# Optimization experiments

Measured on AMD Instinct MI355X. Metric: run time of the kernel, lower is better.

## Reference

```python
import jax, jax.numpy as jnp
import numpy as np

N_COARSE = 64  # n_coarse samples per ray
EPS = 1e-8
DELTA_INF = 1e10


def setup_inputs() -> dict:
    key = jax.random.key(0)
    ks = jax.random.split(key, 8)
    B, H = 16384, 256
    near = 2.0 + jax.random.uniform(ks[0], (B, 1), dtype=jnp.float32)
    far = 6.0 + jax.random.uniform(ks[1], (B, 1), dtype=jnp.float32)
    center = jax.random.normal(ks[2], (B, 3), dtype=jnp.float32)
    direction = jax.random.normal(ks[3], (B, 3), dtype=jnp.float32)
    direction = direction / jnp.linalg.norm(direction, axis=-1, keepdims=True)
    # stand-in NeRF field: 3 -> 256 -> 256 -> 4 MLP (rgb + sigma)
    W1 = jax.random.normal(ks[4], (3, H), dtype=jnp.float32) * 0.5
    b1 = jnp.zeros((H,), jnp.float32)
    W2 = jax.random.normal(ks[5], (H, H), dtype=jnp.float32) * (1.0 / np.sqrt(H))
    b2 = jnp.zeros((H,), jnp.float32)
    W3 = jax.random.normal(ks[6], (H, 4), dtype=jnp.float32) * (1.0 / np.sqrt(H))
    b3 = jnp.zeros((4,), jnp.float32)
    return {"near": near, "far": far, "center": center, "direction": direction,
            "W1": W1, "b1": b1, "W2": W2, "b2": b2, "W3": W3, "b3": b3}


def reference(near, far, center, direction, W1, b1, W2, b2, W3, b3):
    B = near.shape[0]
    K = N_COARSE
    # sample_coarse: stratified z values, lindisp=False, perturb=0
    z_steps = jnp.linspace(0.0, 1.0, K, dtype=near.dtype)[None, :]          # (1, K)
    z_vals = near * (1.0 - z_steps) + far * z_steps                          # (B, K)
    # composite(): deltas with infinite last interval
    deltas = jnp.concatenate(
        [z_vals[:, 1:] - z_vals[:, :-1],
         jnp.full((B, 1), DELTA_INF, dtype=z_vals.dtype)], axis=-1)          # (B, K)
    # world-space sample points along each ray
    points = center[:, None, :] + z_vals[:, :, None] * direction[:, None, :]  # (B, K, 3)
    # model(points) -> (B, K, 4): rgb + sigma
    h = jax.nn.relu(points @ W1 + b1)
    h = jax.nn.relu(h @ W2 + b2)
    out = h @ W3 + b3
    rgbs = out[..., :3]                                                      # (B, K, 3)
    sigmas = out[..., 3]                                                     # (B, K)
    sigmas_last = sigmas[:, -1]
    # alpha compositing (noise_std=0, training=False -> no noise)
    alphas = 1.0 - jnp.exp(-deltas * jax.nn.relu(sigmas))                    # (B, K)
    alphas_shifted = jnp.concatenate(
        [jnp.ones((B, 1), alphas.dtype), 1.0 - alphas + EPS], axis=-1)       # (B, K+1)
    T = jnp.cumprod(alphas_shifted, axis=-1)                                 # transmittance
    weights = alphas * T[:, :-1]                                             # (B, K)
    rgb_final = jnp.sum(weights[..., None] * rgbs, axis=-2)                  # (B, 3)
    depth_final = jnp.sum(weights * z_vals, axis=-1)                         # (B,)
    # white background: rgb += 1 - accumulated alpha
    pix_alpha = jnp.sum(weights, axis=1)
    rgb_final = rgb_final + 1.0 - pix_alpha[:, None]
    return rgb_final, depth_final, weights, sigmas_last
```

## Files before the change

kernel.cpp:

```cpp
#include <hip/hip_runtime.h>
#include <hip/hip_bf16.h>


constexpr int H  = 256;
constexpr int KS = 64;

typedef __attribute__((ext_vector_type(8))) short short8;
typedef __attribute__((ext_vector_type(4))) float f32x4;

__device__ __forceinline__ f32x4 mfma16(short8 a, short8 b, f32x4 c) {
    return __builtin_amdgcn_mfma_f32_16x16x32_bf16(a, b, c, 0, 0, 0);
}
__device__ __forceinline__ void split_bf16(float x, short& hi, short& lo) {
    __hip_bfloat16 h = __float2bfloat16(x);
    float hf = __bfloat162float(h);
    __hip_bfloat16 l = __float2bfloat16(x - hf);
    union { __hip_bfloat16 b; short s; } c1, c2;
    c1.b = h; c2.b = l;
    hi = c1.s; lo = c2.s;
}
__device__ __forceinline__ unsigned short f2bf(float x) {
    union { __hip_bfloat16 b; unsigned short s; } c;
    c.b = __float2bfloat16(x);
    return c.s;
}
__device__ __forceinline__ float bf2f(unsigned short s) {
    union { unsigned int u; float f; } c;
    c.u = ((unsigned int)s) << 16;
    return c.f;
}
__device__ __forceinline__ unsigned int pack2bf(float a, float b) {
    return (unsigned int)f2bf(a) | ((unsigned int)f2bf(b) << 16);
}

__global__ void pack_w2_kernel(const float* __restrict__ W2,
                               unsigned short* __restrict__ hi,
                               unsigned short* __restrict__ lo)
{
    const int i  = blockIdx.x * 256 + threadIdx.x;
    const int e  = i & 7;
    const int l  = (i >> 3) & 63;
    const int nt = (i >> 9) & 15;
    const int ks = i >> 13;
    const int k  = ks * 32 + (l >> 4) * 8 + e;
    const int n  = nt * 16 + (l & 15);
    short h, lw;
    split_bf16(W2[k * H + n], h, lw);
    hi[i] = (unsigned short)h;
    lo[i] = (unsigned short)lw;
}

struct R2a { unsigned short al3[8 * 64 * 8]; };
struct R2b { float comb[8][KS][4]; };
union  R2  { R2a a; R2b b; };
struct SM {
    union { unsigned short ah[8 * 4 * 64 * 8];
            unsigned short h2f[8 * 4 * 64 * 8]; } big;
    R2 r2;
};

__launch_bounds__(512, 8)
__global__ void nerf_mfma_kernel(
    const float* __restrict__ g_near, const float* __restrict__ g_far,
    const float* __restrict__ g_center, const float* __restrict__ g_dir,
    const float* __restrict__ W1, const float* __restrict__ b1,
    const float* __restrict__ b2,
    const float* __restrict__ W3, const float* __restrict__ b3,
    const unsigned short* __restrict__ w2h, const unsigned short* __restrict__ w2l,
    float* __restrict__ out, int B)
{
    __shared__ __align__(16) SM sm;

    const int t    = threadIdx.x;
    const int lane = t & 63;
    const int wv   = __builtin_amdgcn_readfirstlane(t >> 6);
    const int r    = blockIdx.x;

    const float nr = g_near[r], fa = g_far[r];
    const float cx = g_center[r*3+0], cy = g_center[r*3+1], cz = g_center[r*3+2];
    const float dx = g_dir[r*3+0],    dy = g_dir[r*3+1],    dz = g_dir[r*3+2];

    {
        const int kbase = wv * 32 + (lane >> 4) * 8;
        float w1r[3][8], b1r[8];
        #pragma unroll
        for (int c = 0; c < 3; ++c) {
            const f32x4 a = *(const f32x4*)&W1[c * H + kbase];
            const f32x4 b = *(const f32x4*)&W1[c * H + kbase + 4];
            #pragma unroll
            for (int e = 0; e < 4; ++e) { w1r[c][e] = a[e]; w1r[c][e+4] = b[e]; }
        }
        {
            const f32x4 a = *(const f32x4*)&b1[kbase];
            const f32x4 b = *(const f32x4*)&b1[kbase + 4];
            #pragma unroll
            for (int e = 0; e < 4; ++e) { b1r[e] = a[e]; b1r[e+4] = b[e]; }
        }
        const int prow = lane & 15;
        #pragma unroll
        for (int mt = 0; mt < 4; ++mt) {
            const int srow = mt * 16 + prow;
            const float uu = (float)srow * (1.0f / 63.0f);
            const float z  = nr * (1.0f - uu) + fa * uu;
            const float px = cx + z * dx, py = cy + z * dy, pz = cz + z * dz;
            float xs[8];
            #pragma unroll
            for (int e = 0; e < 8; ++e) {
                float x = fmaf(px, w1r[0][e],
                          fmaf(py, w1r[1][e],
                          fmaf(pz, w1r[2][e], b1r[e])));
                xs[e] = fmaxf(x, 0.0f);
            }
            unsigned int hw[4];
            #pragma unroll
            for (int p2 = 0; p2 < 4; ++p2) hw[p2] = pack2bf(xs[p2*2], xs[p2*2+1]);
            *(unsigned int*)&sm.big.ah[((wv*4+mt)*64+lane)*8 + 0] = hw[0];
            *(unsigned int*)&sm.big.ah[((wv*4+mt)*64+lane)*8 + 2] = hw[1];
            *(unsigned int*)&sm.big.ah[((wv*4+mt)*64+lane)*8 + 4] = hw[2];
            *(unsigned int*)&sm.big.ah[((wv*4+mt)*64+lane)*8 + 6] = hw[3];
            if (mt == 3) {
                unsigned int lw[4];
                #pragma unroll
                for (int p2 = 0; p2 < 4; ++p2) {
                    const float l0 = xs[p2*2]   - bf2f((unsigned short)(hw[p2] & 0xffffu));
                    const float l1 = xs[p2*2+1] - bf2f((unsigned short)(hw[p2] >> 16));
                    lw[p2] = pack2bf(l0, l1);
                }
                *(unsigned int*)&sm.r2.a.al3[(wv*64+lane)*8 + 0] = lw[0];
                *(unsigned int*)&sm.r2.a.al3[(wv*64+lane)*8 + 2] = lw[1];
                *(unsigned int*)&sm.r2.a.al3[(wv*64+lane)*8 + 4] = lw[2];
                *(unsigned int*)&sm.r2.a.al3[(wv*64+lane)*8 + 6] = lw[3];
            }
        }
    }
    __syncthreads();

    f32x4 acc[4][2];
    #pragma unroll
    for (int mt = 0; mt < 4; ++mt) {
        acc[mt][0] = (f32x4){0.f,0.f,0.f,0.f};
        acc[mt][1] = (f32x4){0.f,0.f,0.f,0.f};
    }
    {
        const int ntg0 = wv * 2, ntg1 = ntg0 + 1;
        const short8* Bh = (const short8*)w2h;
        const short8* Bl = (const short8*)w2l;
        const short8* Ah = (const short8*)sm.big.ah;
        const short8* Al = (const short8*)sm.r2.a.al3;
        __builtin_amdgcn_s_setprio(1);
        #pragma unroll
        for (int ks = 0; ks < 8; ++ks) {
            const short8 b0h  = Bh[(ks * 16 + ntg0) * 64 + lane];
            const short8 b1h_ = Bh[(ks * 16 + ntg1) * 64 + lane];
            #pragma unroll
            for (int mt = 0; mt < 4; ++mt) {
                const short8 ah = Ah[(ks * 4 + mt) * 64 + lane];
                f32x4 c0 = acc[mt][0], c1 = acc[mt][1];
                c0 = mfma16(ah, b0h, c0);
                c1 = mfma16(ah, b1h_, c1);
                if (mt == 3) {
                    const short8 b0l = Bl[(ks * 16 + ntg0) * 64 + lane];
                    const short8 b1l = Bl[(ks * 16 + ntg1) * 64 + lane];
                    const short8 al  = Al[ks * 64 + lane];
                    c0 = mfma16(ah, b0l, c0);
                    c0 = mfma16(al, b0h, c0);
                    c1 = mfma16(ah, b1l, c1);
                    c1 = mfma16(al, b1h_, c1);
                }
                acc[mt][0] = c0; acc[mt][1] = c1;
            }
        }
        __builtin_amdgcn_s_setprio(0);
    }
    __syncthreads();

    const int  j0 = lane & 15;
    const int  c0 = wv * 32 + j0;
    const int  c1 = c0 + 16;
    const bool lastGrp = ((lane >> 4) == 3);
    float r63a = 0.f, r63b = 0.f;
    {
        const float b2c0 = b2[c0], b2c1 = b2[c1];
        const int rlow = (lane >> 4) * 4;
        const int hi2  = j0 >> 2;
        const int e0   = (j0 & 3) * 2;
        #pragma unroll
        for (int mt = 0; mt < 4; ++mt) {
            const f32x4 v0 = acc[mt][0], v1 = acc[mt][1];
            #pragma unroll
            for (int q = 0; q < 4; ++q) {
                const float a0 = fmaxf(v0[q] + b2c0, 0.0f);
                const float a1 = fmaxf(v1[q] + b2c1, 0.0f);
                const int l2 = (hi2 << 4) | (rlow + q);
                *(unsigned int*)&sm.big.h2f[((wv*4+mt)*64 + l2)*8 + e0] = pack2bf(a0, a1);
                if (mt == 3 && q == 3) { r63a = a0; r63b = a1; }
            }
        }
    }

    {
        const int n  = lane & 15;
        const int hi = lane >> 4;
        short8 bw3;
        #pragma unroll
        for (int e = 0; e < 8; ++e) {
            const int k = wv * 32 + (e & 1) * 16 + hi * 4 + (e >> 1);
            const float v = (n < 4) ? W3[k * 4 + n] : 0.0f;
            bw3[e] = (short)f2bf(v);
        }
        const short8* Ah2 = (const short8*)sm.big.h2f;
        #pragma unroll
        for (int mt = 0; mt < 4; ++mt) {
            const short8 a = Ah2[(wv * 4 + mt) * 64 + lane];
            f32x4 d = (f32x4){0.f,0.f,0.f,0.f};
            d = mfma16(a, bw3, d);
            if (n < 4) {
                #pragma unroll
                for (int q = 0; q < 4; ++q)
                    sm.r2.b.comb[wv][mt * 16 + hi * 4 + q][n] = d[q];
            }
        }
        if (lastGrp) {
            float p = fmaf(r63a, W3[c0 * 4 + 3], r63b * W3[c1 * 4 + 3]);
            #pragma unroll
            for (int off = 1; off < 16; off <<= 1) p += __shfl_xor(p, off, 64);
            if (j0 == 0) sm.r2.b.comb[wv][63][3] = p;
        }
    }
    __syncthreads();

    if (t < KS) {
        const int s = t;

        f32x4 oo = (f32x4){0.f,0.f,0.f,0.f};
        #pragma unroll
        for (int q = 0; q < 8; ++q) {
            const f32x4 c = *(const f32x4*)&sm.r2.b.comb[q][s][0];
            oo[0] += c[0]; oo[1] += c[1]; oo[2] += c[2]; oo[3] += c[3];
        }
        const float o0 = oo[0] + b3[0];
        const float o1 = oo[1] + b3[1];
        const float o2 = oo[2] + b3[2];
        const float sigma = oo[3] + b3[3];

        const float uu = (float)s * (1.0f / 63.0f);
        const float z  = nr * (1.0f - uu) + fa * uu;
        const float u2 = (float)(s + 1) * (1.0f / 63.0f);
        const float z2 = nr * (1.0f - u2) + fa * u2;
        const float delta = (s == 63) ? 1e10f : (z2 - z);
        const float alpha = 1.0f - __expf(-delta * fmaxf(sigma, 0.0f));

        float P = 1.0f - alpha + 1e-8f;
        #pragma unroll
        for (int off = 1; off < 64; off <<= 1) {
            const float v = __shfl_up(P, off, 64);
            if (s >= off) P *= v;
        }
        float T = __shfl_up(P, 1, 64);
        if (s == 0) T = 1.0f;
        const float w = alpha * T;

        out[(size_t)B * 4 + (size_t)r * 64 + s] = w;

        float ws = w, dep = w * z, q0 = w * o0, q1 = w * o1, q2 = w * o2;
        #pragma unroll
        for (int off = 32; off > 0; off >>= 1) {
            ws  += __shfl_xor(ws,  off, 64);
            dep += __shfl_xor(dep, off, 64);
            q0  += __shfl_xor(q0,  off, 64);
            q1  += __shfl_xor(q1,  off, 64);
            q2  += __shfl_xor(q2,  off, 64);
        }
        const float sl = __shfl(sigma, 63, 64);
        if (s == 0) {
            out[(size_t)r * 3 + 0] = q0 + 1.0f - ws;
            out[(size_t)r * 3 + 1] = q1 + 1.0f - ws;
            out[(size_t)r * 3 + 2] = q2 + 1.0f - ws;
            out[(size_t)B * 3 + r] = dep;
            out[(size_t)B * 68 + r] = sl;
        }
    }
}

extern "C" void kernel_launch(void* const* d_in, const int* in_sizes, int n_in,
                              void* d_out, int out_size, void* d_ws, size_t ws_size,
                              hipStream_t stream)
{
    const int B = in_sizes[0];
    if (ws_size < (size_t)(2 * 65536 * sizeof(unsigned short))) return;

    unsigned short* w2h = (unsigned short*)d_ws;
    unsigned short* w2l = w2h + 65536;

    pack_w2_kernel<<<256, 256, 0, stream>>>((const float*)d_in[6], w2h, w2l);

    nerf_mfma_kernel<<<B, 512, 0, stream>>>(
        (const float*)d_in[0], (const float*)d_in[1],
        (const float*)d_in[2], (const float*)d_in[3],
        (const float*)d_in[4], (const float*)d_in[5],
        (const float*)d_in[7],
        (const float*)d_in[8], (const float*)d_in[9],
        w2h, w2l,
        (float*)d_out, B);
}
```

Baseline: 243.9 us.

## Process two rays per block with double-buffered LDS and interleaved phases

Each block now handles two rays, using separate LDS buffers so that layer-1 compute and the layer-2 MFMA for one ray can overlap with work on the other. This cuts the number of barriers per ray and amortises per-block setup such as the W3 fragment, the b2 loads and the W2 tile loads. b2 is now folded into the accumulator initial value, and the setprio calls are removed. In exchange, LDS per block roughly doubles and launch bounds drop to 4 blocks per CU, which may lower occupancy.

New measurement: 461.0 us. +89.0%, slower.

```diff
diff --git a/kernel.cpp b/kernel.cpp
--- a/kernel.cpp
+++ b/kernel.cpp
@@ -50,16 +50,14 @@
     lo[i] = (unsigned short)lw;
 }
 
-struct R2a { unsigned short al3[8 * 64 * 8]; };
-struct R2b { float comb[8][KS][4]; };
-union  R2  { R2a a; R2b b; };
 struct SM {
-    union { unsigned short ah[8 * 4 * 64 * 8];
-            unsigned short h2f[8 * 4 * 64 * 8]; } big;
-    R2 r2;
+    unsigned short A0[8 * 4 * 64 * 8];
+    unsigned short A1[8 * 4 * 64 * 8];
+    unsigned short L0[8 * 64 * 8];
+    unsigned short L1[8 * 64 * 8];
 };
 
-__launch_bounds__(512, 8)
+__launch_bounds__(512, 4)
 __global__ void nerf_mfma_kernel(
     const float* __restrict__ g_near, const float* __restrict__ g_far,
     const float* __restrict__ g_center, const float* __restrict__ g_dir,
@@ -74,12 +72,36 @@
     const int t    = threadIdx.x;
     const int lane = t & 63;
     const int wv   = __builtin_amdgcn_readfirstlane(t >> 6);
-    const int r    = blockIdx.x;
-
-    const float nr = g_near[r], fa = g_far[r];
-    const float cx = g_center[r*3+0], cy = g_center[r*3+1], cz = g_center[r*3+2];
-    const float dx = g_dir[r*3+0],    dy = g_dir[r*3+1],    dz = g_dir[r*3+2];
-
+    const int r0   = blockIdx.x * 2;
+    const int r1g  = r0 + 1;
+    const int r1   = min(r1g, B - 1);
+
+    const float nr0 = g_near[r0], fa0 = g_far[r0];
+    const float nr1 = g_near[r1], fa1 = g_far[r1];
+    const float c0x = g_center[r0*3+0], c0y = g_center[r0*3+1], c0z = g_center[r0*3+2];
+    const float d0x = g_dir[r0*3+0],    d0y = g_dir[r0*3+1],    d0z = g_dir[r0*3+2];
+    const float c1x = g_center[r1*3+0], c1y = g_center[r1*3+1], c1z = g_center[r1*3+2];
+    const float d1x = g_dir[r1*3+0],    d1y = g_dir[r1*3+1],    d1z = g_dir[r1*3+2];
+
+    const int  j0 = lane & 15;
+    const int  cA = wv * 32 + j0, cB = cA + 16;
+    const float b2cA = b2[cA], b2cB = b2[cB];
+    const float w3A = W3[cA * 4 + 3], w3B = W3[cB * 4 + 3];
+    const bool lastGrp = ((lane >> 4) == 3);
+
+    short8 bw3;
+    {
+        const int hi = lane >> 4;
+        #pragma unroll
+        for (int e = 0; e < 8; ++e) {
+            const int k = wv * 32 + (e & 1) * 16 + hi * 4 + (e >> 1);
+            bw3[e] = (short)f2bf((j0 < 4) ? W3[k * 4 + j0] : 0.0f);
+        }
+    }
+
+    auto ph1 = [&](float nr, float fa, float cx, float cy, float cz,
+                   float dx, float dy, float dz,
+                   unsigned short* __restrict__ A, unsigned short* __restrict__ AL3)
     {
         const int kbase = wv * 32 + (lane >> 4) * 8;
         float w1r[3][8], b1r[8];
@@ -114,10 +136,8 @@
             unsigned int hw[4];
             #pragma unroll
             for (int p2 = 0; p2 < 4; ++p2) hw[p2] = pack2bf(xs[p2*2], xs[p2*2+1]);
-            *(unsigned int*)&sm.big.ah[((wv*4+mt)*64+lane)*8 + 0] = hw[0];
-            *(unsigned int*)&sm.big.ah[((wv*4+mt)*64+lane)*8 + 2] = hw[1];
-            *(unsigned int*)&sm.big.ah[((wv*4+mt)*64+lane)*8 + 4] = hw[2];
-            *(unsigned int*)&sm.big.ah[((wv*4+mt)*64+lane)*8 + 6] = hw[3];
+            unsigned int* dst = (unsigned int*)&A[((wv*4+mt)*64+lane)*8];
+            dst[0] = hw[0]; dst[1] = hw[1]; dst[2] = hw[2]; dst[3] = hw[3];
             if (mt == 3) {
                 unsigned int lw[4];
                 #pragma unroll
@@ -126,28 +146,21 @@
                     const float l1 = xs[p2*2+1] - bf2f((unsigned short)(hw[p2] >> 16));
                     lw[p2] = pack2bf(l0, l1);
                 }
-                *(unsigned int*)&sm.r2.a.al3[(wv*64+lane)*8 + 0] = lw[0];
-                *(unsigned int*)&sm.r2.a.al3[(wv*64+lane)*8 + 2] = lw[1];
-                *(unsigned int*)&sm.r2.a.al3[(wv*64+lane)*8 + 4] = lw[2];
-                *(unsigned int*)&sm.r2.a.al3[(wv*64+lane)*8 + 6] = lw[3];
-            }
-        }
-    }
-    __syncthreads();
-
-    f32x4 acc[4][2];
-    #pragma unroll
-    for (int mt = 0; mt < 4; ++mt) {
-        acc[mt][0] = (f32x4){0.f,0.f,0.f,0.f};
-        acc[mt][1] = (f32x4){0.f,0.f,0.f,0.f};
-    }
+                unsigned int* dl = (unsigned int*)&AL3[(wv*64+lane)*8];
+                dl[0] = lw[0]; dl[1] = lw[1]; dl[2] = lw[2]; dl[3] = lw[3];
+            }
+        }
+    };
+
+    auto ph2 = [&](const unsigned short* __restrict__ A,
+                   const unsigned short* __restrict__ AL3,
+                   f32x4 (&acc)[4][2])
     {
         const int ntg0 = wv * 2, ntg1 = ntg0 + 1;
         const short8* Bh = (const short8*)w2h;
         const short8* Bl = (const short8*)w2l;
-        const short8* Ah = (const short8*)sm.big.ah;
-        const short8* Al = (const short8*)sm.r2.a.al3;
-        __builtin_amdgcn_s_setprio(1);
+        const short8* Ah = (const short8*)A;
+        const short8* Al = (const short8*)AL3;
         #pragma unroll
         for (int ks = 0; ks < 8; ++ks) {
             const short8 b0h  = Bh[(ks * 16 + ntg0) * 64 + lane];
@@ -170,17 +183,11 @@
                 acc[mt][0] = c0; acc[mt][1] = c1;
             }
         }
-        __builtin_amdgcn_s_setprio(0);
-    }
-    __syncthreads();
-
-    const int  j0 = lane & 15;
-    const int  c0 = wv * 32 + j0;
-    const int  c1 = c0 + 16;
-    const bool lastGrp = ((lane >> 4) == 3);
-    float r63a = 0.f, r63b = 0.f;
-    {
-        const float b2c0 = b2[c0], b2c1 = b2[c1];
+    };
+
+    auto ph3 = [&](const f32x4 (&acc)[4][2], unsigned short* __restrict__ H2F,
+                   float& r63a, float& r63b)
+    {
         const int rlow = (lane >> 4) * 4;
         const int hi2  = j0 >> 2;
         const int e0   = (j0 & 3) * 2;
@@ -189,97 +196,129 @@
             const f32x4 v0 = acc[mt][0], v1 = acc[mt][1];
             #pragma unroll
             for (int q = 0; q < 4; ++q) {
-                const float a0 = fmaxf(v0[q] + b2c0, 0.0f);
-                const float a1 = fmaxf(v1[q] + b2c1, 0.0f);
+                const float a0 = fmaxf(v0[q], 0.0f);
+                const float a1 = fmaxf(v1[q], 0.0f);
                 const int l2 = (hi2 << 4) | (rlow + q);
-                *(unsigned int*)&sm.big.h2f[((wv*4+mt)*64 + l2)*8 + e0] = pack2bf(a0, a1);
+                *(unsigned int*)&H2F[((wv*4+mt)*64 + l2)*8 + e0] = pack2bf(a0, a1);
                 if (mt == 3 && q == 3) { r63a = a0; r63b = a1; }
             }
         }
-    }
-
-    {
-        const int n  = lane & 15;
+    };
+
+    auto ph4 = [&](const unsigned short* __restrict__ H2F,
+                   float* __restrict__ COMB, float r63a, float r63b)
+    {
         const int hi = lane >> 4;
-        short8 bw3;
-        #pragma unroll
-        for (int e = 0; e < 8; ++e) {
-            const int k = wv * 32 + (e & 1) * 16 + hi * 4 + (e >> 1);
-            const float v = (n < 4) ? W3[k * 4 + n] : 0.0f;
-            bw3[e] = (short)f2bf(v);
-        }
-        const short8* Ah2 = (const short8*)sm.big.h2f;
+        const short8* Ah2 = (const short8*)H2F;
         #pragma unroll
         for (int mt = 0; mt < 4; ++mt) {
             const short8 a = Ah2[(wv * 4 + mt) * 64 + lane];
             f32x4 d = (f32x4){0.f,0.f,0.f,0.f};
             d = mfma16(a, bw3, d);
-            if (n < 4) {
+            if (j0 < 4) {
                 #pragma unroll
                 for (int q = 0; q < 4; ++q)
-                    sm.r2.b.comb[wv][mt * 16 + hi * 4 + q][n] = d[q];
+                    COMB[(wv * 64 + mt * 16 + hi * 4 + q) * 4 + j0] = d[q];
             }
         }
         if (lastGrp) {
-            float p = fmaf(r63a, W3[c0 * 4 + 3], r63b * W3[c1 * 4 + 3]);
+            float p = fmaf(r63a, w3A, r63b * w3B);
             #pragma unroll
             for (int off = 1; off < 16; off <<= 1) p += __shfl_xor(p, off, 64);
-            if (j0 == 0) sm.r2.b.comb[wv][63][3] = p;
-        }
-    }
+            if (j0 == 0) COMB[(wv * 64 + 63) * 4 + 3] = p;
+        }
+    };
+
+    auto ph5 = [&](const float* __restrict__ COMB, float nr, float fa, int r)
+    {
+        if (t < KS) {
+            const int s = t;
+            f32x4 oo = (f32x4){0.f,0.f,0.f,0.f};
+            #pragma unroll
+            for (int q = 0; q < 8; ++q) {
+                const f32x4 c = *(const f32x4*)&COMB[(q * 64 + s) * 4];
+                oo[0] += c[0]; oo[1] += c[1]; oo[2] += c[2]; oo[3] += c[3];
+            }
+            const float o0 = oo[0] + b3[0];
+            const float o1 = oo[1] + b3[1];
+            const float o2 = oo[2] + b3[2];
+            const float sigma = oo[3] + b3[3];
+
+            const float uu = (float)s * (1.0f / 63.0f);
+            const float z  = nr * (1.0f - uu) + fa * uu;
+            const float u2 = (float)(s + 1) * (1.0f / 63.0f);
+            const float z2 = nr * (1.0f - u2) + fa * u2;
+            const float delta = (s == 63) ? 1e10f : (z2 - z);
+            const float alpha = 1.0f - __expf(-delta * fmaxf(sigma, 0.0f));
+
+            float P = 1.0f - alpha + 1e-8f;
+            #pragma unroll
+            for (int off = 1; off < 64; off <<= 1) {
+                const float v = __shfl_up(P, off, 64);
+                if (s >= off) P *= v;
+            }
+            float T = __shfl_up(P, 1, 64);
+            if (s == 0) T = 1.0f;
+            const float w = alpha * T;
+
+            out[(size_t)B * 4 + (size_t)r * 64 + s] = w;
+
+            float ws = w, dep = w * z, q0 = w * o0, q1 = w * o1, q2 = w * o2;
+            #pragma unroll
+            for (int off = 32; off > 0; off >>= 1) {
+                ws  += __shfl_xor(ws,  off, 64);
+                dep += __shfl_xor(dep, off, 64);
+                q0  += __shfl_xor(q0,  off, 64);
+                q1  += __shfl_xor(q1,  off, 64);
+                q2  += __shfl_xor(q2,  off, 64);
+            }
+            const float sl = __shfl(sigma, 63, 64);
+            if (s == 0) {
+                out[(size_t)r * 3 + 0] = q0 + 1.0f - ws;
+                out[(size_t)r * 3 + 1] = q1 + 1.0f - ws;
+                out[(size_t)r * 3 + 2] = q2 + 1.0f - ws;
+                out[(size_t)B * 3 + r] = dep;
+                out[(size_t)B * 68 + r] = sl;
+            }
+        }
+    };
+
+    ph1(nr0, fa0, c0x, c0y, c0z, d0x, d0y, d0z, sm.A0, sm.L0);
     __syncthreads();
 
-    if (t < KS) {
-        const int s = t;
-
-        f32x4 oo = (f32x4){0.f,0.f,0.f,0.f};
-        #pragma unroll
-        for (int q = 0; q < 8; ++q) {
-            const f32x4 c = *(const f32x4*)&sm.r2.b.comb[q][s][0];
-            oo[0] += c[0]; oo[1] += c[1]; oo[2] += c[2]; oo[3] += c[3];
-        }
-        const float o0 = oo[0] + b3[0];
-        const float o1 = oo[1] + b3[1];
-        const float o2 = oo[2] + b3[2];
-        const float sigma = oo[3] + b3[3];
-
-        const float uu = (float)s * (1.0f / 63.0f);
-        const float z  = nr * (1.0f - uu) + fa * uu;
-        const float u2 = (float)(s + 1) * (1.0f / 63.0f);
-        const float z2 = nr * (1.0f - u2) + fa * u2;
-        const float delta = (s == 63) ? 1e10f : (z2 - z);
-        const float alpha = 1.0f - __expf(-delta * fmaxf(sigma, 0.0f));
-
-        float P = 1.0f - alpha + 1e-8f;
-        #pragma unroll
-        for (int off = 1; off < 64; off <<= 1) {
-            const float v = __shfl_up(P, off, 64);
-            if (s >= off) P *= v;
-        }
-        float T = __shfl_up(P, 1, 64);
-        if (s == 0) T = 1.0f;
-        const float w = alpha * T;
-
-        out[(size_t)B * 4 + (size_t)r * 64 + s] = w;
-
-        float ws = w, dep = w * z, q0 = w * o0, q1 = w * o1, q2 = w * o2;
-        #pragma unroll
-        for (int off = 32; off > 0; off >>= 1) {
-            ws  += __shfl_xor(ws,  off, 64);
-            dep += __shfl_xor(dep, off, 64);
-            q0  += __shfl_xor(q0,  off, 64);
-            q1  += __shfl_xor(q1,  off, 64);
-            q2  += __shfl_xor(q2,  off, 64);
-        }
-        const float sl = __shfl(sigma, 63, 64);
-        if (s == 0) {
-            out[(size_t)r * 3 + 0] = q0 + 1.0f - ws;
-            out[(size_t)r * 3 + 1] = q1 + 1.0f - ws;
-            out[(size_t)r * 3 + 2] = q2 + 1.0f - ws;
-            out[(size_t)B * 3 + r] = dep;
-            out[(size_t)B * 68 + r] = sl;
-        }
-    }
+    f32x4 acc0[4][2];
+    #pragma unroll
+    for (int mt = 0; mt < 4; ++mt) {
+        acc0[mt][0] = (f32x4){b2cA, b2cA, b2cA, b2cA};
+        acc0[mt][1] = (f32x4){b2cB, b2cB, b2cB, b2cB};
+    }
+    ph2(sm.A0, sm.L0, acc0);
+    ph1(nr1, fa1, c1x, c1y, c1z, d1x, d1y, d1z, sm.A1, sm.L1);
+    __syncthreads();
+
+    f32x4 acc1[4][2];
+    #pragma unroll
+    for (int mt = 0; mt < 4; ++mt) {
+        acc1[mt][0] = (f32x4){b2cA, b2cA, b2cA, b2cA};
+        acc1[mt][1] = (f32x4){b2cB, b2cB, b2cB, b2cB};
+    }
+    ph2(sm.A1, sm.L1, acc1);
+    {
+        float r63a0 = 0.f, r63b0 = 0.f;
+        ph3(acc0, sm.A0, r63a0, r63b0);
+        ph4(sm.A0, (float*)sm.L0, r63a0, r63b0);
+    }
+    __syncthreads();
+
+    {
+        float r63a1 = 0.f, r63b1 = 0.f;
+        ph3(acc1, sm.A1, r63a1, r63b1);
+        ph4(sm.A1, (float*)sm.L1, r63a1, r63b1);
+    }
+    ph5((const float*)sm.L0, nr0, fa0, r0);
+    __syncthreads();
+
+    if (r1g < B) ph5((const float*)sm.L1, nr1, fa1, r1g);
 }
 
 extern "C" void kernel_launch(void* const* d_in, const int* in_sizes, int n_in,
@@ -294,7 +333,8 @@
 
     pack_w2_kernel<<<256, 256, 0, stream>>>((const float*)d_in[6], w2h, w2l);
 
-    nerf_mfma_kernel<<<B, 512, 0, stream>>>(
+    const int grid = (B + 1) / 2;
+    nerf_mfma_kernel<<<grid, 512, 0, stream>>>(
         (const float*)d_in[0], (const float*)d_in[1],
         (const float*)d_in[2], (const float*)d_in[3],
         (const float*)d_in[4], (const float*)d_in[5],
```
